# Optimization experiments

Hardware: AMD Instinct MI355X
Metric: run time of the kernel (lower is better)

## Reference

```python
import jax, jax.numpy as jnp
import numpy as np

G = 16        # num_groups = num_features // num_channels
CG = 16       # channels per group (num_channels)
EPS = 1e-3


def setup_inputs() -> dict:
    key = jax.random.key(0)
    k1, = jax.random.split(key, 1)
    N, C, H, W = 64, 256, 56, 56
    X = jax.random.normal(k1, (N, C, H, W), dtype=jnp.float32)
    weight = jnp.ones((1, C, 1, 1), dtype=jnp.float32)
    bias = jnp.zeros((1, C, 1, 1), dtype=jnp.float32)
    return {"X": X, "weight": weight, "bias": bias}


def reference(X, weight, bias):
    N, C, H, W = X.shape
    # [N,C,H,W] -> [C, N*H*W] -> groups [G, CG, m]
    x = jnp.transpose(X, (1, 0, 2, 3)).reshape(G, CG, -1)
    m = x.shape[-1]
    mean = jnp.mean(x, axis=-1, keepdims=True)            # [G, CG, 1]
    xc = x - mean                                          # [G, CG, m]
    # sigma = eps*I + (1/m) * xc @ xc^T   (per group)
    sigma = EPS * jnp.eye(CG, dtype=X.dtype) + jnp.einsum('gcm,gdm->gcd', xc, xc) / m
    u, eig, _ = jnp.linalg.svd(sigma)                      # symmetric PSD -> SVD == eig-decomp
    # wm = u @ diag(eig^-1/2) @ u^T
    wm = jnp.einsum('gcd,gd,ged->gce', u, jax.lax.rsqrt(eig), u)  # [G, CG, CG]
    xn = jnp.einsum('gce,gem->gcm', wm, xc)                # whitened
    Xn = xn.reshape(C, N, H, W).transpose(1, 0, 2, 3)      # back to [N,C,H,W]
    return Xn * weight + bias
```

## Files before the change

### kernel.cpp

```cpp
#include <hip/hip_runtime.h>

#define NG   16
#define CG   16
#define NB   64
#define CC   256
#define HW   3136
#define HW4  784
#define MTOT (NB*HW)
#define Q4   (NB*HW4)
#define EPSV 1e-3f
#define NTRI 136
#define NRED (CG+NTRI)

typedef float vfloat4 __attribute__((ext_vector_type(4)));

#define WS_CROSS 256
#define WS_WMW   2432
#define WS_OB    6528

#define SBLK 16
#define TPG  (SBLK*256)
#define FULL_IT 12

__global__ __launch_bounds__(256, 1) void stats_kernel(const float* __restrict__ X,
                                                       float* __restrict__ ws) {
    const int g   = blockIdx.y;
    const int tid = threadIdx.x;
    const float4* __restrict__ X4 = (const float4*)X;
    const int q0  = blockIdx.x * 256 + tid;
    const int gq  = g * CG * HW4;

    float cross[NTRI];
    float csum[CG];
#pragma unroll
    for (int i = 0; i < NTRI; ++i) cross[i] = 0.f;
#pragma unroll
    for (int c = 0; c < CG; ++c) csum[c] = 0.f;

    float4 va[CG], vb[CG];

#define LOADV(V, QQ)                                                       \
    {                                                                      \
        const int q4_ = (QQ);                                              \
        const int n_  = q4_ / HW4;                                         \
        const int p4_ = q4_ - n_ * HW4;                                    \
        const float4* __restrict__ pp_ = X4 + n_ * (CC * HW4) + gq + p4_;  \
        _Pragma("unroll")                                                  \
        for (int c_ = 0; c_ < CG; ++c_) V[c_] = pp_[c_ * HW4];             \
    }

#define ACCV(V)                                                            \
    {                                                                      \
        _Pragma("unroll")                                                  \
        for (int c_ = 0; c_ < CG; ++c_)                                    \
            csum[c_] += (V[c_].x + V[c_].y) + (V[c_].z + V[c_].w);         \
        int i_ = 0;                                                        \
        _Pragma("unroll")                                                  \
        for (int c_ = 0; c_ < CG; ++c_) {                                  \
            _Pragma("unroll")                                              \
            for (int d_ = c_; d_ < CG; ++d_, ++i_)                         \
                cross[i_] += V[c_].x * V[d_].x + V[c_].y * V[d_].y +       \
                             V[c_].z * V[d_].z + V[c_].w * V[d_].w;        \
        }                                                                  \
    }

    const bool tail = (blockIdx.x < 4);

    LOADV(va, q0);
#pragma unroll 1
    for (int p = 0; p < FULL_IT / 2 - 1; ++p) {
        LOADV(vb, q0 + (2 * p + 1) * TPG);
        ACCV(va);
        LOADV(va, q0 + (2 * p + 2) * TPG);
        ACCV(vb);
    }
    LOADV(vb, q0 + 11 * TPG);
    ACCV(va);
    if (tail) LOADV(va, q0 + FULL_IT * TPG);
    ACCV(vb);
    if (tail) ACCV(va);

#undef LOADV
#undef ACCV

    const int lane = tid & 63;
    const int w    = tid >> 6;
#pragma unroll
    for (int c = 0; c < CG; ++c) {
        float v = csum[c];
        v += __shfl_xor(v, 32); v += __shfl_xor(v, 16); v += __shfl_xor(v, 8);
        v += __shfl_xor(v, 4);  v += __shfl_xor(v, 2);  v += __shfl_xor(v, 1);
        csum[c] = v;
    }
#pragma unroll
    for (int i = 0; i < NTRI; ++i) {
        float v = cross[i];
        v += __shfl_xor(v, 32); v += __shfl_xor(v, 16); v += __shfl_xor(v, 8);
        v += __shfl_xor(v, 4);  v += __shfl_xor(v, 2);  v += __shfl_xor(v, 1);
        cross[i] = v;
    }

    __shared__ float part[4][NRED];
    if (lane == 0) {
#pragma unroll
        for (int c = 0; c < CG; ++c) part[w][c] = csum[c];
#pragma unroll
        for (int i = 0; i < NTRI; ++i) part[w][CG + i] = cross[i];
    }
    __syncthreads();
    if (tid < NRED) {
        float s = part[0][tid] + part[1][tid] + part[2][tid] + part[3][tid];
        if (tid < CG) atomicAdd(&ws[g * CG + tid], s);
        else          atomicAdd(&ws[WS_CROSS + g * NTRI + (tid - CG)], s);
    }
}

__global__ __launch_bounds__(256) void newton_kernel(const float* __restrict__ weight,
                                                     const float* __restrict__ bias,
                                                     float* __restrict__ ws) {
    __shared__ float Y[CG][CG + 1], Z[CG][CG + 1], T[CG][CG + 1];
    __shared__ float mean_s[CG];
    __shared__ float red[256];
    __shared__ float s_norm;

    const int g   = blockIdx.x;
    const int tid = threadIdx.x;
    const int c   = tid >> 4;
    const int d   = tid & 15;

    if (tid < CG) mean_s[tid] = ws[g * CG + tid] * (1.0f / MTOT);
    __syncthreads();

    const int cc = min(c, d), dd = max(c, d);
    const int idx = cc * CG + dd - (cc * (cc + 1)) / 2;
    float sig = ws[WS_CROSS + g * NTRI + idx] * (1.0f / MTOT)
              - mean_s[c] * mean_s[d] + ((c == d) ? EPSV : 0.f);

    red[tid] = sig * sig;
    __syncthreads();
    for (int s = 128; s > 0; s >>= 1) {
        if (tid < s) red[tid] += red[tid + s];
        __syncthreads();
    }
    if (tid == 0) s_norm = sqrtf(red[0]);
    __syncthreads();
    const float s = s_norm;

    Y[c][d] = sig / s;
    Z[c][d] = (c == d) ? 1.f : 0.f;
    __syncthreads();

    for (int itn = 0; itn < 12; ++itn) {
        float t = 0.f;
#pragma unroll
        for (int k = 0; k < CG; ++k) t += Z[c][k] * Y[k][d];
        t = ((c == d) ? 3.f : 0.f) - t;
        __syncthreads();
        T[c][d] = t;
        __syncthreads();
        float yn = 0.f, zn = 0.f;
#pragma unroll
        for (int k = 0; k < CG; ++k) {
            yn += Y[c][k] * T[k][d];
            zn += T[c][k] * Z[k][d];
        }
        __syncthreads();
        Y[c][d] = 0.5f * yn;
        Z[c][d] = 0.5f * zn;
        __syncthreads();
    }

    const float wm  = Z[c][d] / sqrtf(s);
    const float w   = weight[g * CG + c];
    const float wmw = wm * w;
    ws[WS_WMW + g * 256 + c * CG + d] = wmw;

    T[c][d] = wmw * mean_s[d];
    __syncthreads();
    if (d == 0) {
        float acc = 0.f;
#pragma unroll
        for (int k = 0; k < CG; ++k) acc += T[c][k];
        ws[WS_OB + g * CG + c] = bias[g * CG + c] - acc;
    }
}

__global__ __launch_bounds__(256, 4) void apply_kernel(const float* __restrict__ X,
                                                       const float* __restrict__ ws,
                                                       float* __restrict__ out) {
    __shared__ float wmw_s[CG][CG];
    __shared__ float ob_s[CG];

    const int g   = blockIdx.y;
    const int tid = threadIdx.x;

    const int q4 = blockIdx.x * 256 + tid;
    const int n  = q4 / HW4;
    const int p4 = q4 - n * HW4;
    const int base = n * (CC * HW4) + (g * CG) * HW4 + p4;

    const float4* __restrict__ X4 = (const float4*)X;
    vfloat4* __restrict__ O4 = (vfloat4*)out;

    float4 v[CG];
#pragma unroll
    for (int cdx = 0; cdx < CG; ++cdx) v[cdx] = X4[base + cdx * HW4];

    wmw_s[tid >> 4][tid & 15] = ws[WS_WMW + g * 256 + tid];
    if (tid < CG) ob_s[tid] = ws[WS_OB + g * CG + tid];
    __syncthreads();

#pragma unroll
    for (int c = 0; c < CG; ++c) {
        const float o = ob_s[c];
        vfloat4 acc;
        acc.x = o; acc.y = o; acc.z = o; acc.w = o;
#pragma unroll
        for (int d = 0; d < CG; ++d) {
            const float w = wmw_s[c][d];
            acc.x += w * v[d].x; acc.y += w * v[d].y;
            acc.z += w * v[d].z; acc.w += w * v[d].w;
        }
        __builtin_nontemporal_store(acc, &O4[base + c * HW4]);
    }
}

extern "C" void kernel_launch(void* const* d_in, const int* in_sizes, int n_in,
                              void* d_out, int out_size, void* d_ws, size_t ws_size,
                              hipStream_t stream) {
    const float* X      = (const float*)d_in[0];
    const float* weight = (const float*)d_in[1];
    const float* bias   = (const float*)d_in[2];
    float* out = (float*)d_out;
    float* ws  = (float*)d_ws;

    (void)hipMemsetAsync(ws, 0, WS_WMW * sizeof(float), stream);

    dim3 g1(SBLK, NG);
    stats_kernel<<<g1, 256, 0, stream>>>(X, ws);

    newton_kernel<<<NG, 256, 0, stream>>>(weight, bias, ws);

    dim3 g3(196, NG);
    apply_kernel<<<g3, 196 == 196 ? 256 : 256, 0, stream>>>(X, ws, out);
}
```

Measured before the change: 400.0 us.

## Fuse stats, Newton-Schulz and apply into one persistent kernel with grid barriers

Replaces the three separate launches with a single persistent kernel of 256 blocks. The blocks synchronise through atomic grid barriers in workspace memory, and each block reuses its stats-phase slice of X for the double-buffered apply phase. This removes two kernel launch gaps and lets the apply reads hit L2/MALL where possible. The cost is only 256 blocks streaming the apply pass, so occupancy is lower than the old 3136-block apply grid. The barrier also risks deadlock if not all blocks are co-resident, and 240 blocks sit idle while the Newton iteration runs.

```diff
diff --git a/kernel.cpp b/kernel.cpp
--- a/kernel.cpp
+++ b/kernel.cpp
@@ -17,27 +17,58 @@
 #define WS_CROSS 256
 #define WS_WMW   2432
 #define WS_OB    6528
-
-#define SBLK 16
-#define TPG  (SBLK*256)
+#define WS_BAR   6784
+#define WS_ZERO_BYTES ((WS_BAR + 8) * 4)
+
+#define NBLK   256
+#define TPG    4096
 #define FULL_IT 12
 
-__global__ __launch_bounds__(256, 1) void stats_kernel(const float* __restrict__ X,
-                                                       float* __restrict__ ws) {
-    const int g   = blockIdx.y;
+__device__ __forceinline__ void grid_barrier(float* ws, int which) {
+    __syncthreads();
+    if (threadIdx.x == 0) {
+        unsigned* ctr = (unsigned*)(ws + WS_BAR) + which;
+        __threadfence();
+        __hip_atomic_fetch_add(ctr, 1u, __ATOMIC_RELEASE, __HIP_MEMORY_SCOPE_AGENT);
+        while (__hip_atomic_load(ctr, __ATOMIC_ACQUIRE, __HIP_MEMORY_SCOPE_AGENT) < NBLK) {
+            __builtin_amdgcn_s_sleep(2);
+        }
+    }
+    __syncthreads();
+}
+
+__global__ __launch_bounds__(256, 1) void dbn_fused(const float* __restrict__ X,
+                                                    const float* __restrict__ weight,
+                                                    const float* __restrict__ bias,
+                                                    float* __restrict__ out,
+                                                    float* __restrict__ ws) {
+    const int bid = blockIdx.x;
+    const int g   = bid & 15;
+    const int sb  = bid >> 4;
     const int tid = threadIdx.x;
+    const int q0  = sb * 256 + tid;
+    const int gq  = g * CG * HW4;
+    const bool tail = (sb < 4);
+
     const float4* __restrict__ X4 = (const float4*)X;
-    const int q0  = blockIdx.x * 256 + tid;
-    const int gq  = g * CG * HW4;
-
-    float cross[NTRI];
-    float csum[CG];
-#pragma unroll
-    for (int i = 0; i < NTRI; ++i) cross[i] = 0.f;
-#pragma unroll
-    for (int c = 0; c < CG; ++c) csum[c] = 0.f;
-
-    float4 va[CG], vb[CG];
+
+    __shared__ float part[4][NRED];
+    __shared__ float Y[CG][CG + 1], Z[CG][CG + 1], T[CG][CG + 1];
+    __shared__ float mean_s[CG];
+    __shared__ float red[256];
+    __shared__ float s_norm;
+    __shared__ float wmw_s[CG][CG];
+    __shared__ float ob_s[CG];
+
+    {
+        float cross[NTRI];
+        float csum[CG];
+#pragma unroll
+        for (int i = 0; i < NTRI; ++i) cross[i] = 0.f;
+#pragma unroll
+        for (int c = 0; c < CG; ++c) csum[c] = 0.f;
+
+        float4 va[CG], vb[CG];
 
 #define LOADV(V, QQ)                                                       \
     {                                                                      \
@@ -64,164 +95,184 @@
         }                                                                  \
     }
 
-    const bool tail = (blockIdx.x < 4);
-
-    LOADV(va, q0);
+        LOADV(va, q0);
 #pragma unroll 1
-    for (int p = 0; p < FULL_IT / 2 - 1; ++p) {
-        LOADV(vb, q0 + (2 * p + 1) * TPG);
+        for (int p = 0; p < FULL_IT / 2 - 1; ++p) {
+            LOADV(vb, q0 + (2 * p + 1) * TPG);
+            ACCV(va);
+            LOADV(va, q0 + (2 * p + 2) * TPG);
+            ACCV(vb);
+        }
+        LOADV(vb, q0 + 11 * TPG);
         ACCV(va);
-        LOADV(va, q0 + (2 * p + 2) * TPG);
+        if (tail) LOADV(va, q0 + FULL_IT * TPG);
         ACCV(vb);
-    }
-    LOADV(vb, q0 + 11 * TPG);
-    ACCV(va);
-    if (tail) LOADV(va, q0 + FULL_IT * TPG);
-    ACCV(vb);
-    if (tail) ACCV(va);
+        if (tail) ACCV(va);
 
 #undef LOADV
 #undef ACCV
 
-    const int lane = tid & 63;
-    const int w    = tid >> 6;
-#pragma unroll
-    for (int c = 0; c < CG; ++c) {
-        float v = csum[c];
-        v += __shfl_xor(v, 32); v += __shfl_xor(v, 16); v += __shfl_xor(v, 8);
-        v += __shfl_xor(v, 4);  v += __shfl_xor(v, 2);  v += __shfl_xor(v, 1);
-        csum[c] = v;
-    }
-#pragma unroll
-    for (int i = 0; i < NTRI; ++i) {
-        float v = cross[i];
-        v += __shfl_xor(v, 32); v += __shfl_xor(v, 16); v += __shfl_xor(v, 8);
-        v += __shfl_xor(v, 4);  v += __shfl_xor(v, 2);  v += __shfl_xor(v, 1);
-        cross[i] = v;
-    }
-
-    __shared__ float part[4][NRED];
-    if (lane == 0) {
-#pragma unroll
-        for (int c = 0; c < CG; ++c) part[w][c] = csum[c];
-#pragma unroll
-        for (int i = 0; i < NTRI; ++i) part[w][CG + i] = cross[i];
-    }
-    __syncthreads();
-    if (tid < NRED) {
-        float s = part[0][tid] + part[1][tid] + part[2][tid] + part[3][tid];
-        if (tid < CG) atomicAdd(&ws[g * CG + tid], s);
-        else          atomicAdd(&ws[WS_CROSS + g * NTRI + (tid - CG)], s);
-    }
-}
-
-__global__ __launch_bounds__(256) void newton_kernel(const float* __restrict__ weight,
-                                                     const float* __restrict__ bias,
-                                                     float* __restrict__ ws) {
-    __shared__ float Y[CG][CG + 1], Z[CG][CG + 1], T[CG][CG + 1];
-    __shared__ float mean_s[CG];
-    __shared__ float red[256];
-    __shared__ float s_norm;
-
-    const int g   = blockIdx.x;
-    const int tid = threadIdx.x;
-    const int c   = tid >> 4;
-    const int d   = tid & 15;
-
-    if (tid < CG) mean_s[tid] = ws[g * CG + tid] * (1.0f / MTOT);
-    __syncthreads();
-
-    const int cc = min(c, d), dd = max(c, d);
-    const int idx = cc * CG + dd - (cc * (cc + 1)) / 2;
-    float sig = ws[WS_CROSS + g * NTRI + idx] * (1.0f / MTOT)
-              - mean_s[c] * mean_s[d] + ((c == d) ? EPSV : 0.f);
-
-    red[tid] = sig * sig;
-    __syncthreads();
-    for (int s = 128; s > 0; s >>= 1) {
-        if (tid < s) red[tid] += red[tid + s];
-        __syncthreads();
-    }
-    if (tid == 0) s_norm = sqrtf(red[0]);
-    __syncthreads();
-    const float s = s_norm;
-
-    Y[c][d] = sig / s;
-    Z[c][d] = (c == d) ? 1.f : 0.f;
-    __syncthreads();
-
-    for (int itn = 0; itn < 12; ++itn) {
-        float t = 0.f;
-#pragma unroll
-        for (int k = 0; k < CG; ++k) t += Z[c][k] * Y[k][d];
-        t = ((c == d) ? 3.f : 0.f) - t;
-        __syncthreads();
-        T[c][d] = t;
-        __syncthreads();
-        float yn = 0.f, zn = 0.f;
-#pragma unroll
-        for (int k = 0; k < CG; ++k) {
-            yn += Y[c][k] * T[k][d];
-            zn += T[c][k] * Z[k][d];
-        }
-        __syncthreads();
-        Y[c][d] = 0.5f * yn;
-        Z[c][d] = 0.5f * zn;
-        __syncthreads();
-    }
-
-    const float wm  = Z[c][d] / sqrtf(s);
-    const float w   = weight[g * CG + c];
-    const float wmw = wm * w;
-    ws[WS_WMW + g * 256 + c * CG + d] = wmw;
-
-    T[c][d] = wmw * mean_s[d];
-    __syncthreads();
-    if (d == 0) {
-        float acc = 0.f;
-#pragma unroll
-        for (int k = 0; k < CG; ++k) acc += T[c][k];
-        ws[WS_OB + g * CG + c] = bias[g * CG + c] - acc;
-    }
-}
-
-__global__ __launch_bounds__(256, 4) void apply_kernel(const float* __restrict__ X,
-                                                       const float* __restrict__ ws,
-                                                       float* __restrict__ out) {
-    __shared__ float wmw_s[CG][CG];
-    __shared__ float ob_s[CG];
-
-    const int g   = blockIdx.y;
-    const int tid = threadIdx.x;
-
-    const int q4 = blockIdx.x * 256 + tid;
-    const int n  = q4 / HW4;
-    const int p4 = q4 - n * HW4;
-    const int base = n * (CC * HW4) + (g * CG) * HW4 + p4;
-
-    const float4* __restrict__ X4 = (const float4*)X;
-    vfloat4* __restrict__ O4 = (vfloat4*)out;
-
-    float4 v[CG];
-#pragma unroll
-    for (int cdx = 0; cdx < CG; ++cdx) v[cdx] = X4[base + cdx * HW4];
-
-    wmw_s[tid >> 4][tid & 15] = ws[WS_WMW + g * 256 + tid];
-    if (tid < CG) ob_s[tid] = ws[WS_OB + g * CG + tid];
-    __syncthreads();
-
-#pragma unroll
-    for (int c = 0; c < CG; ++c) {
-        const float o = ob_s[c];
-        vfloat4 acc;
-        acc.x = o; acc.y = o; acc.z = o; acc.w = o;
-#pragma unroll
-        for (int d = 0; d < CG; ++d) {
-            const float w = wmw_s[c][d];
-            acc.x += w * v[d].x; acc.y += w * v[d].y;
-            acc.z += w * v[d].z; acc.w += w * v[d].w;
-        }
-        __builtin_nontemporal_store(acc, &O4[base + c * HW4]);
+        const int lane = tid & 63;
+        const int w    = tid >> 6;
+#pragma unroll
+        for (int c = 0; c < CG; ++c) {
+            float v = csum[c];
+            v += __shfl_xor(v, 32); v += __shfl_xor(v, 16); v += __shfl_xor(v, 8);
+            v += __shfl_xor(v, 4);  v += __shfl_xor(v, 2);  v += __shfl_xor(v, 1);
+            csum[c] = v;
+        }
+#pragma unroll
+        for (int i = 0; i < NTRI; ++i) {
+            float v = cross[i];
+            v += __shfl_xor(v, 32); v += __shfl_xor(v, 16); v += __shfl_xor(v, 8);
+            v += __shfl_xor(v, 4);  v += __shfl_xor(v, 2);  v += __shfl_xor(v, 1);
+            cross[i] = v;
+        }
+
+        if (lane == 0) {
+#pragma unroll
+            for (int c = 0; c < CG; ++c) part[w][c] = csum[c];
+#pragma unroll
+            for (int i = 0; i < NTRI; ++i) part[w][CG + i] = cross[i];
+        }
+        __syncthreads();
+        if (tid < NRED) {
+            float s = part[0][tid] + part[1][tid] + part[2][tid] + part[3][tid];
+            if (tid < CG) atomicAdd(&ws[g * CG + tid], s);
+            else          atomicAdd(&ws[WS_CROSS + g * NTRI + (tid - CG)], s);
+        }
+    }
+
+    grid_barrier(ws, 0);
+
+    if (bid < NG) {
+        const int gg = bid;
+        const int c  = tid >> 4;
+        const int d  = tid & 15;
+
+        if (tid < CG)
+            mean_s[tid] = __hip_atomic_load(&ws[gg * CG + tid], __ATOMIC_RELAXED,
+                                            __HIP_MEMORY_SCOPE_AGENT) * (1.0f / MTOT);
+        __syncthreads();
+
+        const int cc = min(c, d), dd = max(c, d);
+        const int idx = cc * CG + dd - (cc * (cc + 1)) / 2;
+        float sig = __hip_atomic_load(&ws[WS_CROSS + gg * NTRI + idx], __ATOMIC_RELAXED,
+                                      __HIP_MEMORY_SCOPE_AGENT) * (1.0f / MTOT)
+                  - mean_s[c] * mean_s[d] + ((c == d) ? EPSV : 0.f);
+
+        red[tid] = sig * sig;
+        __syncthreads();
+        for (int s = 128; s > 0; s >>= 1) {
+            if (tid < s) red[tid] += red[tid + s];
+            __syncthreads();
+        }
+        if (tid == 0) s_norm = sqrtf(red[0]);
+        __syncthreads();
+        const float s = s_norm;
+
+        Y[c][d] = sig / s;
+        Z[c][d] = (c == d) ? 1.f : 0.f;
+        __syncthreads();
+
+        for (int itn = 0; itn < 12; ++itn) {
+            float t = 0.f;
+#pragma unroll
+            for (int k = 0; k < CG; ++k) t += Z[c][k] * Y[k][d];
+            t = ((c == d) ? 3.f : 0.f) - t;
+            __syncthreads();
+            T[c][d] = t;
+            __syncthreads();
+            float yn = 0.f, zn = 0.f;
+#pragma unroll
+            for (int k = 0; k < CG; ++k) {
+                yn += Y[c][k] * T[k][d];
+                zn += T[c][k] * Z[k][d];
+            }
+            __syncthreads();
+            Y[c][d] = 0.5f * yn;
+            Z[c][d] = 0.5f * zn;
+            __syncthreads();
+        }
+
+        const float wm  = Z[c][d] / sqrtf(s);
+        const float w   = weight[gg * CG + c];
+        const float wmw = wm * w;
+        __hip_atomic_store(&ws[WS_WMW + gg * 256 + c * CG + d], wmw,
+                           __ATOMIC_RELAXED, __HIP_MEMORY_SCOPE_AGENT);
+
+        T[c][d] = wmw * mean_s[d];
+        __syncthreads();
+        if (d == 0) {
+            float acc = 0.f;
+#pragma unroll
+            for (int k = 0; k < CG; ++k) acc += T[c][k];
+            __hip_atomic_store(&ws[WS_OB + gg * CG + c], bias[gg * CG + c] - acc,
+                               __ATOMIC_RELAXED, __HIP_MEMORY_SCOPE_AGENT);
+        }
+    }
+
+    grid_barrier(ws, 1);
+
+    {
+        wmw_s[tid >> 4][tid & 15] = __hip_atomic_load(&ws[WS_WMW + g * 256 + tid],
+                                                      __ATOMIC_RELAXED,
+                                                      __HIP_MEMORY_SCOPE_AGENT);
+        if (tid < CG)
+            ob_s[tid] = __hip_atomic_load(&ws[WS_OB + g * CG + tid],
+                                          __ATOMIC_RELAXED, __HIP_MEMORY_SCOPE_AGENT);
+        __syncthreads();
+
+        vfloat4* __restrict__ O4 = (vfloat4*)out;
+        float4 pa[CG], pb[CG];
+
+#define LOADA(V, QQ)                                                       \
+    {                                                                      \
+        const int q4_ = (QQ);                                              \
+        const int n_  = q4_ / HW4;                                         \
+        const int p4_ = q4_ - n_ * HW4;                                    \
+        const float4* __restrict__ pp_ = X4 + n_ * (CC * HW4) + gq + p4_;  \
+        _Pragma("unroll")                                                  \
+        for (int c_ = 0; c_ < CG; ++c_) V[c_] = pp_[c_ * HW4];             \
+    }
+
+#define APPV(V, QQ)                                                        \
+    {                                                                      \
+        const int q4_ = (QQ);                                              \
+        const int n_  = q4_ / HW4;                                         \
+        const int p4_ = q4_ - n_ * HW4;                                    \
+        const int base_ = n_ * (CC * HW4) + gq + p4_;                      \
+        _Pragma("unroll")                                                  \
+        for (int c_ = 0; c_ < CG; ++c_) {                                  \
+            const float o_ = ob_s[c_];                                     \
+            vfloat4 acc_;                                                  \
+            acc_.x = o_; acc_.y = o_; acc_.z = o_; acc_.w = o_;            \
+            _Pragma("unroll")                                              \
+            for (int d_ = 0; d_ < CG; ++d_) {                              \
+                const float w_ = wmw_s[c_][d_];                            \
+                acc_.x += w_ * V[d_].x; acc_.y += w_ * V[d_].y;            \
+                acc_.z += w_ * V[d_].z; acc_.w += w_ * V[d_].w;            \
+            }                                                              \
+            __builtin_nontemporal_store(acc_, &O4[base_ + c_ * HW4]);      \
+        }                                                                  \
+    }
+
+        LOADA(pa, q0);
+#pragma unroll 1
+        for (int p = 0; p < FULL_IT / 2 - 1; ++p) {
+            LOADA(pb, q0 + (2 * p + 1) * TPG);
+            APPV(pa, q0 + (2 * p) * TPG);
+            LOADA(pa, q0 + (2 * p + 2) * TPG);
+            APPV(pb, q0 + (2 * p + 1) * TPG);
+        }
+        LOADA(pb, q0 + 11 * TPG);
+        APPV(pa, q0 + 10 * TPG);
+        if (tail) LOADA(pa, q0 + FULL_IT * TPG);
+        APPV(pb, q0 + 11 * TPG);
+        if (tail) APPV(pa, q0 + FULL_IT * TPG);
+
+#undef LOADA
+#undef APPV
     }
 }
 
@@ -234,13 +285,7 @@
     float* out = (float*)d_out;
     float* ws  = (float*)d_ws;
 
-    (void)hipMemsetAsync(ws, 0, WS_WMW * sizeof(float), stream);
-
-    dim3 g1(SBLK, NG);
-    stats_kernel<<<g1, 256, 0, stream>>>(X, ws);
-
-    newton_kernel<<<NG, 256, 0, stream>>>(weight, bias, ws);
-
-    dim3 g3(196, NG);
-    apply_kernel<<<g3, 196 == 196 ? 256 : 256, 0, stream>>>(X, ws, out);
+    (void)hipMemsetAsync(ws, 0, WS_ZERO_BYTES, stream);
+
+    dbn_fused<<<dim3(NBLK), 256, 0, stream>>>(X, weight, bias, out, ws);
 }
```

Result: slower. 700.0 us (+75.0%).
